# Performance work log

Measured on AMD Instinct MI355X. Metric: run time of the kernel, lower is better.

The kernel has to match this reference:

```python
import jax, jax.numpy as jnp
import numpy as np

B, N, D, H = 4, 8192, 1024, 16
C = D // H  # head dim = 64
EPS = 1e-6


def setup_inputs() -> dict:
    key = jax.random.key(0)
    ks = jax.random.split(key, 8)
    sc = 0.02
    return {
        "q": jax.random.normal(ks[0], (B, N, D), jnp.float32),
        "k": jax.random.normal(ks[1], (B, N, D), jnp.float32),
        "v": jax.random.normal(ks[2], (B, N, D), jnp.float32),
        "Wq": jax.random.normal(ks[3], (D, D), jnp.float32) * sc,
        "Wk": jax.random.normal(ks[4], (D, D), jnp.float32) * sc,
        "Wv": jax.random.normal(ks[5], (D, D), jnp.float32) * sc,
        "Wproj": jax.random.normal(ks[6], (D, D), jnp.float32) * sc,
        "focusing_factor": jnp.asarray(3.0, jnp.float32),
    }


def _to_heads(x):
    # b n (h c) -> (b h) n c
    return x.reshape(B, N, H, C).transpose(0, 2, 1, 3).reshape(B * H, N, C)


def reference(q, k, v, Wq, Wk, Wv, Wproj, focusing_factor):
    # projections (torch Linear: x @ W.T, no bias)
    qp = q @ Wq.T
    kp = k @ Wk.T
    vp = v @ Wv.T

    def feature_map(x):
        # |GELU(x)| + eps, then focused renormalization:
        # softmax(focusing_factor * log(f)) * mean(f)
        f = jnp.abs(jax.nn.gelu(x, approximate=False)) + EPS
        f_norm = f.mean(axis=-1, keepdims=True)
        return jax.nn.softmax(jnp.log(f) * focusing_factor, axis=-1) * f_norm

    qf = feature_map(qp)
    kf = feature_map(kp)

    qh = _to_heads(qf)  # [B*H, N, C]
    kh = _to_heads(kf)
    vh = _to_heads(vp)

    k_mean = kh.mean(axis=1)  # [B*H, C]
    z_inv = jnp.einsum('bnd,bd->bn', qh, k_mean) + EPS  # [B*H, N]

    # (k/sqrt(N))^T (v/sqrt(N)) == (k^T v)/N
    kv = jnp.einsum('bnc,bnd->bcd', kh, vh) / N  # [B*H, C, C]
    y = jnp.einsum('bic,bcd->bid', qh, kv) / z_inv[..., None]  # [B*H, N, C]

    y = y.reshape(B, H, N, C).transpose(0, 2, 1, 3).reshape(B, N, D)
    return y @ Wproj.T
```

## Files before the change

kernel.cpp:

```cpp
#include <hip/hip_runtime.h>

using f16 = _Float16;
typedef __attribute__((ext_vector_type(4))) _Float16 f16x4;
typedef __attribute__((ext_vector_type(8))) _Float16 f16x8;
typedef __attribute__((ext_vector_type(4))) float f32x4;

#define DEVI __device__ __forceinline__

namespace {

constexpr int BB = 4;
constexpr int NN = 8192;
constexpr int DD = 1024;
constexpr int MTOT = BB * NN;
constexpr float FSCALE = 64.0f;
constexpr float ZCONST = 64.0f * 64.0f * (8192.0f * 1e-6f);

DEVI void gl16(const void* g, void* l) {
  __builtin_amdgcn_global_load_lds(
      (__attribute__((address_space(1))) void*)(void*)g,
      (__attribute__((address_space(3))) void*)l, 16, 0, 0);
}

DEVI float wsum(float v) {
#pragma unroll
  for (int m = 32; m > 0; m >>= 1) v += __shfl_xor(v, m, 64);
  return v;
}
DEVI float wmaxr(float v) {
#pragma unroll
  for (int m = 32; m > 0; m >>= 1) v = fmaxf(v, __shfl_xor(v, m, 64));
  return v;
}
DEVI float block_sum(float v, float* sred, int tid) {
  v = wsum(v);
  __syncthreads();
  if ((tid & 63) == 0) sred[tid >> 6] = v;
  __syncthreads();
  return sred[0] + sred[1] + sred[2] + sred[3];
}
DEVI float block_max(float v, float* sred, int tid) {
  v = wmaxr(v);
  __syncthreads();
  if ((tid & 63) == 0) sred[tid >> 6] = v;
  __syncthreads();
  return fmaxf(fmaxf(sred[0], sred[1]), fmaxf(sred[2], sred[3]));
}

struct CastArgs {
  const float* src[8];
  f16* dst[8];
  int n4[8];
};

__global__ __launch_bounds__(256) void cast_kernel(CastArgs a) {
  const int z = blockIdx.y;
  const float4* __restrict__ s = (const float4*)a.src[z];
  f16x4* __restrict__ d = (f16x4*)a.dst[z];
  const int n4 = a.n4[z];
  for (int i = blockIdx.x * blockDim.x + threadIdx.x; i < n4;
       i += gridDim.x * blockDim.x) {
    float4 f = s[i];
    f16x4 o = {(f16)f.x, (f16)f.y, (f16)f.z, (f16)f.w};
    d[i] = o;
  }
}

struct Gemm3 {
  const f16* A[3];
  const f16* Bt[3];
  void* C[3];
};

template <typename OutT>
__global__ __launch_bounds__(256) void gemm_bt(Gemm3 P) {
  constexpr int K = DD;
  constexpr int N = DD;
  const int z = blockIdx.z;
  const f16* __restrict__ A = P.A[z];
  const f16* __restrict__ Bt = P.Bt[z];
  OutT* __restrict__ C = (OutT*)P.C[z];

  const int tid = threadIdx.x;
  const int lane = tid & 63, wave = tid >> 6;
  const size_t row0 = (size_t)blockIdx.y * 128;
  const size_t col0 = (size_t)blockIdx.x * 128;

  __shared__ __align__(16) f16 As[128 * 32];
  __shared__ __align__(16) f16 Bs[128 * 32];

  f32x4 acc[4][4];
#pragma unroll
  for (int i = 0; i < 4; ++i)
#pragma unroll
    for (int j = 0; j < 4; ++j) acc[i][j] = f32x4{0.f, 0.f, 0.f, 0.f};

  const int srow = lane >> 2;
  const int skb = (lane & 3) ^ ((lane >> 3) & 3);
  const int fr = lane & 15;
  const int fkbp = (lane >> 4) ^ ((lane >> 1) & 3);
  const int wr = (wave >> 1) * 64;
  const int wc = (wave & 1) * 64;

  for (int kt = 0; kt < K; kt += 32) {
#pragma unroll
    for (int c = 0; c < 2; ++c) {
      const int r = (wave * 2 + c) * 16 + srow;
      gl16(A + (row0 + r) * K + kt + skb * 8, &As[(wave * 2 + c) * 512]);
      gl16(Bt + (col0 + r) * K + kt + skb * 8, &Bs[(wave * 2 + c) * 512]);
    }
    __syncthreads();
    f16x8 af[4], bf[4];
#pragma unroll
    for (int mi = 0; mi < 4; ++mi)
      af[mi] = *(const f16x8*)&As[(wr + mi * 16 + fr) * 32 + fkbp * 8];
#pragma unroll
    for (int ni = 0; ni < 4; ++ni)
      bf[ni] = *(const f16x8*)&Bs[(wc + ni * 16 + fr) * 32 + fkbp * 8];
#pragma unroll
    for (int mi = 0; mi < 4; ++mi)
#pragma unroll
      for (int ni = 0; ni < 4; ++ni)
        acc[mi][ni] = __builtin_amdgcn_mfma_f32_16x16x32_f16(
            af[mi], bf[ni], acc[mi][ni], 0, 0, 0);
    __syncthreads();
  }

#pragma unroll
  for (int mi = 0; mi < 4; ++mi)
#pragma unroll
    for (int ni = 0; ni < 4; ++ni) {
      const size_t colv = col0 + wc + ni * 16 + fr;
#pragma unroll
      for (int r = 0; r < 4; ++r) {
        const size_t rowv = row0 + wr + mi * 16 + (lane >> 4) * 4 + r;
        C[rowv * N + colv] = (OutT)acc[mi][ni][r];
      }
    }
}

__global__ __launch_bounds__(256) void feature_kernel(
    const f16* __restrict__ qp, const f16* __restrict__ kp,
    f16* __restrict__ qf, f16* __restrict__ kf, const float* __restrict__ ffp) {
  const int row = blockIdx.x;
  const int tid = threadIdx.x;
  const bool isq = (blockIdx.y == 0);
  const f16* __restrict__ src = isq ? qp : kp;
  f16* __restrict__ dst = isq ? qf : kf;
  const float ff = ffp[0];
  __shared__ float sred[4];

  f16x4 xv = ((const f16x4*)src)[(size_t)row * 256 + tid];
  float f0[4];
  float ps = 0.f;
#pragma unroll
  for (int j = 0; j < 4; ++j) {
    float x = (float)xv[j];
    float g = 0.5f * x * (1.0f + erff(x * 0.70710678118654752f));
    float fv = fabsf(g) + 1e-6f;
    f0[j] = fv;
    ps += fv;
  }
  float fsum = block_sum(ps, sred, tid);
  float t[4];
  float pm = -1e30f;
#pragma unroll
  for (int j = 0; j < 4; ++j) {
    t[j] = ff * __logf(f0[j]);
    pm = fmaxf(pm, t[j]);
  }
  float tmax = block_max(pm, sred, tid);
  float e[4];
  float es = 0.f;
#pragma unroll
  for (int j = 0; j < 4; ++j) {
    e[j] = __expf(t[j] - tmax);
    es += e[j];
  }
  float esum = block_sum(es, sred, tid);
  const float scale = fsum * (1.0f / 1024.0f) / esum * FSCALE;
  f16x4 o;
#pragma unroll
  for (int j = 0; j < 4; ++j) o[j] = (f16)(e[j] * scale);
  ((f16x4*)dst)[(size_t)row * 256 + tid] = o;
}

__global__ __launch_bounds__(256) void kv_kernel(
    const f16* __restrict__ kf, const f16* __restrict__ vp,
    float* __restrict__ kvsum, float* __restrict__ colsum) {
  const int bh = blockIdx.x;
  const int b = bh >> 4, h = bh & 15;
  const int tid = threadIdx.x, lane = tid & 63, wave = tid >> 6;
  __shared__ __align__(16) f16 kt[32 * 64];
  __shared__ __align__(16) f16 vt[32 * 64];
  __shared__ float csred[4][64];

  f32x4 acc[4];
#pragma unroll
  for (int ni = 0; ni < 4; ++ni) acc[ni] = f32x4{0.f, 0.f, 0.f, 0.f};
  float cpart = 0.f;

  const int srow = wave * 8 + (lane >> 3);
  const int scol = (lane & 7) * 8;
  const int colbase = h * 64;
  const int n0base = blockIdx.y * 512;

  for (int n0 = n0base; n0 < n0base + 512; n0 += 32) {
    const size_t gofs = ((size_t)(b * NN + n0 + srow)) * DD + colbase + scol;
    gl16(kf + gofs, &kt[wave * 512]);
    gl16(vp + gofs, &vt[wave * 512]);
    __syncthreads();
    {
      const int c = tid & 63;
      const int r0 = (tid >> 6) * 8;
#pragma unroll
      for (int rr = 0; rr < 8; ++rr) cpart += (float)kt[(r0 + rr) * 64 + c];
    }
    f16x8 a, bfr[4];
#pragma unroll
    for (int j = 0; j < 8; ++j)
      a[j] = kt[((lane >> 4) * 8 + j) * 64 + wave * 16 + (lane & 15)];
#pragma unroll
    for (int ni = 0; ni < 4; ++ni)
#pragma unroll
      for (int j = 0; j < 8; ++j)
        bfr[ni][j] = vt[((lane >> 4) * 8 + j) * 64 + ni * 16 + (lane & 15)];
#pragma unroll
    for (int ni = 0; ni < 4; ++ni)
      acc[ni] = __builtin_amdgcn_mfma_f32_16x16x32_f16(a, bfr[ni], acc[ni], 0, 0, 0);
    __syncthreads();
  }
#pragma unroll
  for (int ni = 0; ni < 4; ++ni)
#pragma unroll
    for (int r = 0; r < 4; ++r) {
      const int c = wave * 16 + (lane >> 4) * 4 + r;
      const int d = ni * 16 + (lane & 15);
      atomicAdd(&kvsum[(size_t)bh * 4096 + c * 64 + d], acc[ni][r]);
    }
  csred[tid >> 6][tid & 63] = cpart;
  __syncthreads();
  if (tid < 64)
    atomicAdd(&colsum[bh * 64 + tid],
              csred[0][tid] + csred[1][tid] + csred[2][tid] + csred[3][tid]);
}

__global__ __launch_bounds__(256) void y_kernel(
    const f16* __restrict__ qf, const f16* __restrict__ kv16,
    const float* __restrict__ colsum, f16* __restrict__ y) {
  const int bh = blockIdx.x, b = bh >> 4, h = bh & 15;
  const int n0 = blockIdx.y * 128;
  const int tid = threadIdx.x, lane = tid & 63, wave = tid >> 6;
  __shared__ __align__(16) f16 qs[128 * 64];
  __shared__ __align__(16) f16 kvs[64 * 64];
  __shared__ float cs[64];
  __shared__ float zr[128];

#pragma unroll
  for (int cc = 0; cc < 4; ++cc) {
    const int r = wave * 32 + cc * 8 + (lane >> 3);
    gl16(qf + ((size_t)(b * NN + n0 + r)) * DD + h * 64 + (lane & 7) * 8,
         &qs[(wave * 4 + cc) * 512]);
  }
#pragma unroll
  for (int cc = 0; cc < 2; ++cc) {
    const int r = wave * 16 + cc * 8 + (lane >> 3);
    gl16(kv16 + (size_t)bh * 4096 + r * 64 + (lane & 7) * 8,
         &kvs[(wave * 2 + cc) * 512]);
  }
  if (tid < 64) cs[tid] = colsum[bh * 64 + tid];
  __syncthreads();
  if (tid < 128) {
    float zv = 0.f;
    for (int cc = 0; cc < 64; ++cc) {
      const int c = (cc + tid) & 63;
      zv += (float)qs[tid * 64 + c] * cs[c];
    }
    zr[tid] = zv + ZCONST;
  }
  __syncthreads();

  f32x4 acc[2][4];
#pragma unroll
  for (int mi = 0; mi < 2; ++mi)
#pragma unroll
    for (int ni = 0; ni < 4; ++ni) acc[mi][ni] = f32x4{0.f, 0.f, 0.f, 0.f};

#pragma unroll
  for (int ks = 0; ks < 2; ++ks) {
    f16x8 a[2], bfr[4];
#pragma unroll
    for (int mi = 0; mi < 2; ++mi)
      a[mi] = *(const f16x8*)&qs[(wave * 32 + mi * 16 + (lane & 15)) * 64 +
                                 ks * 32 + (lane >> 4) * 8];
#pragma unroll
    for (int ni = 0; ni < 4; ++ni)
#pragma unroll
      for (int j = 0; j < 8; ++j)
        bfr[ni][j] = kvs[(ks * 32 + (lane >> 4) * 8 + j) * 64 + ni * 16 + (lane & 15)];
#pragma unroll
    for (int mi = 0; mi < 2; ++mi)
#pragma unroll
      for (int ni = 0; ni < 4; ++ni)
        acc[mi][ni] = __builtin_amdgcn_mfma_f32_16x16x32_f16(
            a[mi], bfr[ni], acc[mi][ni], 0, 0, 0);
  }
#pragma unroll
  for (int mi = 0; mi < 2; ++mi)
#pragma unroll
    for (int ni = 0; ni < 4; ++ni)
#pragma unroll
      for (int r = 0; r < 4; ++r) {
        const int rrow = wave * 32 + mi * 16 + (lane >> 4) * 4 + r;
        const int d = ni * 16 + (lane & 15);
        const float yv = acc[mi][ni][r] / zr[rrow];
        y[((size_t)(b * NN + n0 + rrow)) * DD + h * 64 + d] = (f16)yv;
      }
}

}

extern "C" void kernel_launch(void* const* d_in, const int* in_sizes, int n_in,
                              void* d_out, int out_size, void* d_ws, size_t ws_size,
                              hipStream_t stream) {
  const float* q = (const float*)d_in[0];
  const float* k = (const float*)d_in[1];
  const float* v = (const float*)d_in[2];
  const float* Wq = (const float*)d_in[3];
  const float* Wk = (const float*)d_in[4];
  const float* Wv = (const float*)d_in[5];
  const float* Wp = (const float*)d_in[6];
  const float* ffp = (const float*)d_in[7];

  char* w = (char*)d_ws;
  size_t off = 0;
  auto alloc = [&](size_t b) {
    void* p = (void*)(w + off);
    off += (b + 255) & ~(size_t)255;
    return p;
  };
  const size_t big = (size_t)MTOT * DD * sizeof(f16);
  f16* q16 = (f16*)alloc(big);
  f16* k16 = (f16*)alloc(big);
  f16* v16 = (f16*)alloc(big);
  f16* qp16 = (f16*)alloc(big);
  f16* kp16 = (f16*)alloc(big);
  f16* vp16 = (f16*)alloc(big);
  f16* Wq16 = (f16*)alloc((size_t)DD * DD * 2);
  f16* Wk16 = (f16*)alloc((size_t)DD * DD * 2);
  f16* Wv16 = (f16*)alloc((size_t)DD * DD * 2);
  f16* Wp16 = (f16*)alloc((size_t)DD * DD * 2);
  float* kvsum = (float*)alloc(64 * 64 * 64 * sizeof(float));
  float* colsum = (float*)alloc(64 * 64 * sizeof(float));
  f16* kv16 = (f16*)alloc(64 * 64 * 64 * sizeof(f16));
  if (off > ws_size) return;

  f16* qf = q16;
  f16* kf = k16;
  f16* y16 = v16;

  CastArgs ca{};
  ca.src[0] = q;  ca.dst[0] = q16;  ca.n4[0] = MTOT * DD / 4;
  ca.src[1] = k;  ca.dst[1] = k16;  ca.n4[1] = MTOT * DD / 4;
  ca.src[2] = v;  ca.dst[2] = v16;  ca.n4[2] = MTOT * DD / 4;
  ca.src[3] = Wq; ca.dst[3] = Wq16; ca.n4[3] = DD * DD / 4;
  ca.src[4] = Wk; ca.dst[4] = Wk16; ca.n4[4] = DD * DD / 4;
  ca.src[5] = Wv; ca.dst[5] = Wv16; ca.n4[5] = DD * DD / 4;
  ca.src[6] = Wp; ca.dst[6] = Wp16; ca.n4[6] = DD * DD / 4;
  cast_kernel<<<dim3(1024, 7), 256, 0, stream>>>(ca);

  Gemm3 gp{};
  gp.A[0] = q16; gp.Bt[0] = Wq16; gp.C[0] = qp16;
  gp.A[1] = k16; gp.Bt[1] = Wk16; gp.C[1] = kp16;
  gp.A[2] = v16; gp.Bt[2] = Wv16; gp.C[2] = vp16;
  gemm_bt<f16><<<dim3(DD / 128, MTOT / 128, 3), 256, 0, stream>>>(gp);

  feature_kernel<<<dim3(MTOT, 2), 256, 0, stream>>>(qp16, kp16, qf, kf, ffp);

  hipMemsetAsync(kvsum, 0, 64 * 64 * 64 * sizeof(float) + 64 * 64 * sizeof(float),
                 stream);
  kv_kernel<<<dim3(64, 16), 256, 0, stream>>>(kf, vp16, kvsum, colsum);

  CastArgs cb{};
  cb.src[0] = kvsum; cb.dst[0] = kv16; cb.n4[0] = 64 * 64 * 64 / 4;
  cast_kernel<<<dim3(64, 1), 256, 0, stream>>>(cb);

  y_kernel<<<dim3(64, 64), 256, 0, stream>>>(qf, kv16, colsum, y16);

  Gemm3 gf{};
  gf.A[0] = y16; gf.Bt[0] = Wp16; gf.C[0] = d_out;
  gemm_bt<float><<<dim3(DD / 128, MTOT / 128, 1), 256, 0, stream>>>(gf);
}
```

Measured before the change: 723.1 us.

## Replace 128x128 GEMM with double-buffered 256x256 tile kernel

Replaces the simple 128x128 tile GEMM, which loads one K-slice and syncs twice per step, with a 256x256 tile, 512-thread kernel. It double-buffers LDS over K=64 slices and issues async global-to-LDS loads for the next slices between MFMA phases. It also uses s_setprio around the MFMA bursts and swizzles the block index to group blocks for better L2 reuse. The aim is to hide load latency and raise MFMA utilisation in the projection GEMMs, which dominate runtime. In exchange it needs 128KB of LDS per block and hand-placed waitcnt and barrier sequencing, which is fragile to get right.

```diff
diff --git a/kernel.cpp b/kernel.cpp
--- a/kernel.cpp
+++ b/kernel.cpp
@@ -73,67 +73,140 @@
 };
 
 template <typename OutT>
-__global__ __launch_bounds__(256) void gemm_bt(Gemm3 P) {
+__global__ __launch_bounds__(512, 2) void gemm256(Gemm3 P) {
   constexpr int K = DD;
   constexpr int N = DD;
+  constexpr int NKT = K / 64;
   const int z = blockIdx.z;
   const f16* __restrict__ A = P.A[z];
   const f16* __restrict__ Bt = P.Bt[z];
   OutT* __restrict__ C = (OutT*)P.C[z];
 
-  const int tid = threadIdx.x;
-  const int lane = tid & 63, wave = tid >> 6;
-  const size_t row0 = (size_t)blockIdx.y * 128;
-  const size_t col0 = (size_t)blockIdx.x * 128;
-
-  __shared__ __align__(16) f16 As[128 * 32];
-  __shared__ __align__(16) f16 Bs[128 * 32];
-
-  f32x4 acc[4][4];
-#pragma unroll
-  for (int i = 0; i < 4; ++i)
+  const int nx = gridDim.x;
+  int lin = blockIdx.y * nx + blockIdx.x;
+  const int cpx = (gridDim.y * nx) >> 3;
+  lin = (lin & 7) * cpx + (lin >> 3);
+  const size_t row0 = (size_t)(lin / nx) * 256;
+  const size_t col0 = (size_t)(lin % nx) * 256;
+
+  const int tid = threadIdx.x, lane = tid & 63, wv = tid >> 6;
+  const int wm = wv >> 2, wn = wv & 3;
+  const int fr = lane & 15, f7 = lane & 7, kq = lane >> 4;
+
+  __shared__ __align__(16) f16 LA[2][2][8192];
+  __shared__ __align__(16) f16 LB[2][2][8192];
+
+  const int srow = wv * 8 + (lane >> 3);
+  const int ssw = (lane & 7) ^ ((lane >> 3) & 7);
+
+  auto stageA = [&](int kts, int half) {
+    const f16* src = A + (row0 + half * 128 + srow) * K + kts * 64 + ssw * 8;
+    f16* dst = &LA[kts & 1][half][wv * 512];
+#pragma unroll
+    for (int c = 0; c < 2; ++c) gl16(src + (size_t)c * 64 * K, dst + c * 4096);
+  };
+  auto stageB = [&](int kts, int half) {
+    const f16* src = Bt + (col0 + half * 128 + srow) * K + kts * 64 + ssw * 8;
+    f16* dst = &LB[kts & 1][half][wv * 512];
+#pragma unroll
+    for (int c = 0; c < 2; ++c) gl16(src + (size_t)c * 64 * K, dst + c * 4096);
+  };
+
+  f32x4 acc[8][4];
+#pragma unroll
+  for (int i = 0; i < 8; ++i)
 #pragma unroll
     for (int j = 0; j < 4; ++j) acc[i][j] = f32x4{0.f, 0.f, 0.f, 0.f};
 
-  const int srow = lane >> 2;
-  const int skb = (lane & 3) ^ ((lane >> 3) & 3);
-  const int fr = lane & 15;
-  const int fkbp = (lane >> 4) ^ ((lane >> 1) & 3);
-  const int wr = (wave >> 1) * 64;
-  const int wc = (wave & 1) * 64;
-
-  for (int kt = 0; kt < K; kt += 32) {
-#pragma unroll
-    for (int c = 0; c < 2; ++c) {
-      const int r = (wave * 2 + c) * 16 + srow;
-      gl16(A + (row0 + r) * K + kt + skb * 8, &As[(wave * 2 + c) * 512]);
-      gl16(Bt + (col0 + r) * K + kt + skb * 8, &Bs[(wave * 2 + c) * 512]);
-    }
-    __syncthreads();
-    f16x8 af[4], bf[4];
-#pragma unroll
-    for (int mi = 0; mi < 4; ++mi)
-      af[mi] = *(const f16x8*)&As[(wr + mi * 16 + fr) * 32 + fkbp * 8];
-#pragma unroll
-    for (int ni = 0; ni < 4; ++ni)
-      bf[ni] = *(const f16x8*)&Bs[(wc + ni * 16 + fr) * 32 + fkbp * 8];
+  stageA(0, 0); stageA(0, 1); stageB(0, 0); stageB(0, 1);
+  stageA(1, 0); stageA(1, 1);
+  asm volatile("s_waitcnt vmcnt(4)" ::: "memory");
+  __builtin_amdgcn_s_barrier();
+
+  const int c0e = (kq ^ f7) * 8;
+#pragma unroll 2
+  for (int kt = 0; kt < NKT; ++kt) {
+    const int buf = kt & 1;
+    const f16* Ah = LA[buf][wm];
+    const f16* Bh = &LB[buf][wn >> 1][(wn & 1) * 4096];
+    f16x8 a0[8], a1[8], b0[4], b1[4];
+
+#pragma unroll
+    for (int mi = 0; mi < 8; ++mi)
+      a0[mi] = *(const f16x8*)&Ah[(mi * 16 + fr) * 64 + c0e];
+#pragma unroll
+    for (int ni = 0; ni < 4; ++ni)
+      b0[ni] = *(const f16x8*)&Bh[(ni * 16 + fr) * 64 + c0e];
+    if (kt < NKT - 1) stageB(kt + 1, 0);
+    __builtin_amdgcn_s_barrier();
+    asm volatile("s_waitcnt lgkmcnt(0)" ::: "memory");
+    __builtin_amdgcn_s_setprio(1);
 #pragma unroll
     for (int mi = 0; mi < 4; ++mi)
 #pragma unroll
       for (int ni = 0; ni < 4; ++ni)
         acc[mi][ni] = __builtin_amdgcn_mfma_f32_16x16x32_f16(
-            af[mi], bf[ni], acc[mi][ni], 0, 0, 0);
-    __syncthreads();
-  }
-
-#pragma unroll
-  for (int mi = 0; mi < 4; ++mi)
+            a0[mi], b0[ni], acc[mi][ni], 0, 0, 0);
+    __builtin_amdgcn_s_setprio(0);
+    __builtin_amdgcn_s_barrier();
+
+#pragma unroll
+    for (int mi = 0; mi < 8; ++mi)
+      a1[mi] = *(const f16x8*)&Ah[(mi * 16 + fr) * 64 + (c0e ^ 32)];
+    if (kt < NKT - 1) stageB(kt + 1, 1);
+    __builtin_amdgcn_s_barrier();
+    asm volatile("s_waitcnt lgkmcnt(0)" ::: "memory");
+    __builtin_amdgcn_s_setprio(1);
+#pragma unroll
+    for (int mi = 4; mi < 8; ++mi)
+#pragma unroll
+      for (int ni = 0; ni < 4; ++ni)
+        acc[mi][ni] = __builtin_amdgcn_mfma_f32_16x16x32_f16(
+            a0[mi], b0[ni], acc[mi][ni], 0, 0, 0);
+    __builtin_amdgcn_s_setprio(0);
+    __builtin_amdgcn_s_barrier();
+
+#pragma unroll
+    for (int ni = 0; ni < 4; ++ni)
+      b1[ni] = *(const f16x8*)&Bh[(ni * 16 + fr) * 64 + (c0e ^ 32)];
+    if (kt < NKT - 2) stageA(kt + 2, 0);
+    __builtin_amdgcn_s_barrier();
+    asm volatile("s_waitcnt lgkmcnt(0)" ::: "memory");
+    __builtin_amdgcn_s_setprio(1);
+#pragma unroll
+    for (int mi = 0; mi < 4; ++mi)
+#pragma unroll
+      for (int ni = 0; ni < 4; ++ni)
+        acc[mi][ni] = __builtin_amdgcn_mfma_f32_16x16x32_f16(
+            a1[mi], b1[ni], acc[mi][ni], 0, 0, 0);
+    __builtin_amdgcn_s_setprio(0);
+    __builtin_amdgcn_s_barrier();
+
+    if (kt < NKT - 2) stageA(kt + 2, 1);
+    __builtin_amdgcn_s_barrier();
+    __builtin_amdgcn_s_setprio(1);
+#pragma unroll
+    for (int mi = 4; mi < 8; ++mi)
+#pragma unroll
+      for (int ni = 0; ni < 4; ++ni)
+        acc[mi][ni] = __builtin_amdgcn_mfma_f32_16x16x32_f16(
+            a1[mi], b1[ni], acc[mi][ni], 0, 0, 0);
+    __builtin_amdgcn_s_setprio(0);
+    if (kt < NKT - 2)
+      asm volatile("s_waitcnt vmcnt(4)" ::: "memory");
+    else
+      asm volatile("s_waitcnt vmcnt(0)" ::: "memory");
+    __builtin_amdgcn_s_barrier();
+  }
+
+#pragma unroll
+  for (int mi = 0; mi < 8; ++mi)
 #pragma unroll
     for (int ni = 0; ni < 4; ++ni) {
-      const size_t colv = col0 + wc + ni * 16 + fr;
+      const size_t colv = col0 + wn * 64 + ni * 16 + fr;
 #pragma unroll
       for (int r = 0; r < 4; ++r) {
-        const size_t rowv = row0 + wr + mi * 16 + (lane >> 4) * 4 + r;
+        const size_t rowv = row0 + wm * 128 + mi * 16 + (lane >> 4) * 4 + r;
         C[rowv * N + colv] = (OutT)acc[mi][ni][r];
       }
     }
@@ -373,7 +446,7 @@
   gp.A[0] = q16; gp.Bt[0] = Wq16; gp.C[0] = qp16;
   gp.A[1] = k16; gp.Bt[1] = Wk16; gp.C[1] = kp16;
   gp.A[2] = v16; gp.Bt[2] = Wv16; gp.C[2] = vp16;
-  gemm_bt<f16><<<dim3(DD / 128, MTOT / 128, 3), 256, 0, stream>>>(gp);
+  gemm256<f16><<<dim3(DD / 256, MTOT / 256, 3), 512, 0, stream>>>(gp);
 
   feature_kernel<<<dim3(MTOT, 2), 256, 0, stream>>>(qp16, kp16, qf, kf, ffp);
 
@@ -389,5 +462,5 @@
 
   Gemm3 gf{};
   gf.A[0] = y16; gf.Bt[0] = Wp16; gf.C[0] = d_out;
-  gemm_bt<float><<<dim3(DD / 128, MTOT / 128, 1), 256, 0, stream>>>(gf);
-}
+  gemm256<float><<<dim3(DD / 256, MTOT / 256, 1), 512, 0, stream>>>(gf);
+}
```

After: 700.3 us. 1.03x faster.
